# Optimization experiments

Hardware: AMD Instinct MI355X
Metric: run time of the kernel (lower is better)

Reference implementation:

```python
import jax, jax.numpy as jnp
import numpy as np

B, C, M, T = 2, 512, 16, 128
H = 8
D = C // H  # 64, divisible by 4 for 2D RoPE
G = C // 4  # GroupNorm groups = 128
S = M * T


def group_norm(x, scale, bias, groups=G, eps=1e-5):
    b, c, m, t = x.shape
    xg = x.reshape(b, groups, c // groups, m, t)
    mu = xg.mean(axis=(2, 3, 4), keepdims=True)
    var = xg.var(axis=(2, 3, 4), keepdims=True)
    xn = ((xg - mu) * jax.lax.rsqrt(var + eps)).reshape(b, c, m, t)
    return xn * scale[None, :, None, None] + bias[None, :, None, None]


def dwsep_conv(x, dw, pw):
    # depthwise 3x3 (groups=C) then pointwise 1x1
    y = jax.lax.conv_general_dilated(
        x, dw, window_strides=(1, 1), padding='SAME',
        dimension_numbers=('NCHW', 'HWIO', 'NCHW'), feature_group_count=x.shape[1])
    return jnp.einsum('bcmt,cd->bdmt', y, pw)


def rope2d(x):
    # x: [B,H,M,T,D]; first D/2 dims rotated by freq index m, last D/2 by time index t
    d = x.shape[-1]
    dh = d // 2
    q = dh // 2
    inv = 1.0 / (10000.0 ** (jnp.arange(q, dtype=jnp.float32) / q))

    def rot(v, ang):
        h = v.shape[-1] // 2
        v1, v2 = v[..., :h], v[..., h:]
        c, s = jnp.cos(ang), jnp.sin(ang)
        return jnp.concatenate([v1 * c - v2 * s, v1 * s + v2 * c], axis=-1)

    ang_f = jnp.arange(x.shape[2], dtype=jnp.float32)[:, None] * inv  # [M,q]
    ang_t = jnp.arange(x.shape[3], dtype=jnp.float32)[:, None] * inv  # [T,q]
    xf = rot(x[..., :dh], ang_f[:, None, :])  # broadcast over T
    xt = rot(x[..., dh:], ang_t)
    return jnp.concatenate([xf, xt], axis=-1)


def setup_inputs() -> dict:
    key = jax.random.key(0)
    ks = jax.random.split(key, 14)
    s = 0.02
    return {
        'x': jax.random.normal(ks[0], (B, C, M, T), jnp.float32),
        'lengths': jax.random.randint(ks[1], (B,), T // 2, T + 1),
        'gn_scale': jnp.ones((C,), jnp.float32),
        'gn_bias': jnp.zeros((C,), jnp.float32),
        'dw_q': jax.random.normal(ks[2], (3, 3, 1, C), jnp.float32) * s,
        'dw_k': jax.random.normal(ks[3], (3, 3, 1, C), jnp.float32) * s,
        'dw_v': jax.random.normal(ks[4], (3, 3, 1, C), jnp.float32) * s,
        'pw_q': jax.random.normal(ks[5], (C, C), jnp.float32) * s,
        'pw_k': jax.random.normal(ks[6], (C, C), jnp.float32) * s,
        'pw_v': jax.random.normal(ks[7], (C, C), jnp.float32) * s,
        'attn_w': jax.random.normal(ks[8], (C, C), jnp.float32) * s,
        'attn_b': jnp.zeros((C,), jnp.float32),
        'out_w': jax.random.normal(ks[9], (C, C), jnp.float32) * s,
        'out_b': jnp.zeros((C,), jnp.float32),
    }


def reference(x, lengths, gn_scale, gn_bias, dw_q, dw_k, dw_v, pw_q, pw_k, pw_v,
              attn_w, attn_b, out_w, out_b):
    residual = x
    xn = group_norm(x, gn_scale, gn_bias)

    def to_heads(y):  # [B,C,M,T] -> [B,H,M,T,D]
        return y.reshape(B, H, D, M, T).transpose(0, 1, 3, 4, 2)

    q = rope2d(to_heads(dwsep_conv(xn, dw_q, pw_q)))
    k = rope2d(to_heads(dwsep_conv(xn, dw_k, pw_k)))
    v = to_heads(dwsep_conv(xn, dw_v, pw_v))

    q = q.reshape(B, H, S, D)
    k = k.reshape(B, H, S, D)
    v = v.reshape(B, H, S, D)

    scores = jnp.einsum('bhsd,bhkd->bhsk', q, k) / np.sqrt(D).astype(np.float32)
    valid_t = jnp.arange(T)[None, :] < lengths[:, None]        # [B,T]
    valid = jnp.tile(valid_t, (1, M))                          # [B,S], token idx = m*T + t
    scores = jnp.where(valid[:, None, None, :], scores, jnp.float32(-1e9))
    attn = jax.nn.softmax(scores, axis=-1)
    o = jnp.einsum('bhsk,bhkd->bhsd', attn, v)                 # [B,H,S,D]

    o = o.transpose(0, 2, 1, 3).reshape(B, S, C)
    o = o @ attn_w + attn_b                                    # block output proj
    o = o.reshape(B, M, T, C).transpose(0, 3, 1, 2)            # [B,C,M,T]
    out = jnp.einsum('bcmt,cd->bdmt', o, out_w) + out_b[None, :, None, None]
    return residual + out
```

## Files before the change

### kernel.cpp

```cpp
#include <hip/hip_runtime.h>
#include <math.h>

#define CCH 512
#define SSQ 2048
#define MTOT 4096

typedef __bf16 bf16;
typedef __bf16 bf16x8 __attribute__((ext_vector_type(8)));
typedef __bf16 bf16x4 __attribute__((ext_vector_type(4)));
typedef float  f32x4  __attribute__((ext_vector_type(4)));

#define AS1 __attribute__((address_space(1)))
#define AS3 __attribute__((address_space(3)))
__device__ __forceinline__ void glds16(const void* g, void* l) {
    __builtin_amdgcn_global_load_lds((const AS1 void*)g, (AS3 void*)l, 16, 0, 0);
}

__global__ __launch_bounds__(256) void gnw_kernel(const float* __restrict__ x,
        float* __restrict__ mu, float* __restrict__ rstd,
        const float* __restrict__ w0, const float* __restrict__ w1,
        const float* __restrict__ w2, const float* __restrict__ w3,
        const float* __restrict__ w4, bf16* __restrict__ wT,
        const float* __restrict__ attnb, const float* __restrict__ outb,
        float* __restrict__ bcv) {
    __shared__ float smem[64*65];
    int tid = threadIdx.x;
    if (blockIdx.x < 256) {
        float* s_sum = smem;
        float* s_sq  = smem + 256;
        int bg = blockIdx.x;
        long base = (long)bg * 8192;
        float sum = 0.f, sq = 0.f;
#pragma unroll
        for (int r = 0; r < 32; ++r) {
            float v = x[base + r*256 + tid];
            sum += v; sq += v*v;
        }
        s_sum[tid] = sum; s_sq[tid] = sq;
        __syncthreads();
        for (int off = 128; off > 0; off >>= 1) {
            if (tid < off) { s_sum[tid] += s_sum[tid+off]; s_sq[tid] += s_sq[tid+off]; }
            __syncthreads();
        }
        if (tid == 0) {
            float m = s_sum[0] * (1.f/8192.f);
            float v = s_sq[0]  * (1.f/8192.f) - m*m;
            mu[bg] = m;
            rstd[bg] = rsqrtf(v + 1e-5f);
        }
    } else if (blockIdx.x < 576) {
        int bid = blockIdx.x - 256;
        int z = bid >> 6, r2 = bid & 63;
        int k0 = (r2 >> 3)*64, n0 = (r2 & 7)*64;
        const float* srcs[5] = {w0, w1, w2, w3, w4};
        const float* W = srcs[z];
        bf16* D = wT + (long)z * (CCH*CCH);
        float (*t)[65] = (float(*)[65])smem;
        int cI = tid & 63, r4 = tid >> 6;
#pragma unroll
        for (int p = 0; p < 16; ++p) {
            int kr = p*4 + r4;
            t[kr][cI] = W[(long)(k0+kr)*CCH + n0 + cI];
        }
        __syncthreads();
#pragma unroll
        for (int p = 0; p < 16; ++p) {
            int nr = p*4 + r4;
            D[(long)(n0+nr)*CCH + k0 + cI] = (bf16)t[cI][nr];
        }
    } else if (blockIdx.x < 578) {
        int n = (blockIdx.x - 576)*256 + tid;
        float a = outb[n];
#pragma unroll 16
        for (int j = 0; j < 512; ++j)
            a = fmaf(attnb[j], w4[(long)j*CCH + n], a);
        bcv[n] = a;
    } else {
        bf16* wAc = wT + (long)5*CCH*CCH;
        int base = (blockIdx.x - 578)*4096 + tid;
#pragma unroll
        for (int p = 0; p < 16; ++p)
            wAc[base + p*256] = (bf16)w3[base + p*256];
    }
}

__global__ void tn_kernel(const float* __restrict__ x, const float* __restrict__ mu,
                          const float* __restrict__ rstd, const float* __restrict__ gsc,
                          const float* __restrict__ gbs, bf16* __restrict__ xnT) {
    __shared__ float t[64][65];
    int s0 = blockIdx.x*64, c0 = blockIdx.y*64, b = blockIdx.z;
    int tid = threadIdx.x;
    int cI = tid & 63, r4 = tid >> 6;
#pragma unroll
    for (int p = 0; p < 16; ++p) {
        int cr = p*4 + r4;
        t[cr][cI] = x[((long)(b*CCH + c0 + cr))*SSQ + s0 + cI];
    }
    __syncthreads();
#pragma unroll
    for (int p = 0; p < 16; ++p) {
        int sr = p*4 + r4;
        int c = c0 + cI;
        int g = b*128 + (c >> 2);
        float v = (t[cI][sr] - mu[g]) * rstd[g] * gsc[c] + gbs[c];
        xnT[((long)(b*SSQ + s0 + sr))*CCH + c] = (bf16)v;
    }
}

__global__ __launch_bounds__(256) void dw3_kernel(const bf16* __restrict__ xnT,
        const float* __restrict__ dwq, const float* __restrict__ dwk,
        const float* __restrict__ dwv,
        bf16* __restrict__ yq, bf16* __restrict__ yk, bf16* __restrict__ yv) {
    int tid = threadIdx.x;
    int cc = (tid & 63) * 8;
    int s  = blockIdx.x*4 + (tid >> 6);
    int sl = s & (SSQ-1);
    int b  = s >> 11;
    int m = sl >> 7, t = sl & 127;
    float aq[8] = {}, ak[8] = {}, av[8] = {};
#pragma unroll
    for (int di = 0; di < 3; ++di) {
        int m2 = m + di - 1;
        if ((unsigned)m2 >= 16u) continue;
#pragma unroll
        for (int dj = 0; dj < 3; ++dj) {
            int t2 = t + dj - 1;
            if ((unsigned)t2 >= 128u) continue;
            bf16x8 xv = *(const bf16x8*)(xnT + ((long)(b*SSQ + m2*128 + t2))*CCH + cc);
            int wi = (di*3 + dj)*CCH + cc;
#pragma unroll
            for (int i = 0; i < 8; ++i) {
                float xf = (float)xv[i];
                aq[i] += xf * dwq[wi+i];
                ak[i] += xf * dwk[wi+i];
                av[i] += xf * dwv[wi+i];
            }
        }
    }
    bf16x8 oq, ok, ov;
#pragma unroll
    for (int i = 0; i < 8; ++i) { oq[i] = (bf16)aq[i]; ok[i] = (bf16)ak[i]; ov[i] = (bf16)av[i]; }
    long o = (long)s*CCH + cc;
    *(bf16x8*)(yq + o) = oq;
    *(bf16x8*)(yk + o) = ok;
    *(bf16x8*)(yv + o) = ov;
}

template<int NFR>
__device__ __forceinline__ void gemm_core128(const bf16* __restrict__ A,
        const bf16* __restrict__ Wt, int m0, int n0,
        bf16* As, bf16* Bs, f32x4 (&acc)[4][NFR]) {
    int tid = threadIdx.x, lane = tid & 63, wid = tid >> 6;
    int sw = wid & 1, nw = wid >> 1;
    int col = lane & 15, quad = lane >> 4;
    const char* gA[4]; char* ldsA[4];
#pragma unroll
    for (int p = 0; p < 4; ++p) {
        int ci = tid + p*256;
        int row = ci >> 3;
        int c = (ci & 7) ^ (row & 7);
        gA[p] = (const char*)A + ((long)(m0+row)*CCH + c*8)*2;
        ldsA[p] = (char*)As + ci*16;
    }
    const char* gB[NFR]; char* ldsB[NFR];
#pragma unroll
    for (int p = 0; p < NFR; ++p) {
        int ci = tid + p*256;
        int row = ci >> 3;
        int c = (ci & 7) ^ (row & 7);
        gB[p] = (const char*)Wt + ((long)(n0+row)*CCH + c*8)*2;
        ldsB[p] = (char*)Bs + ci*16;
    }
    int rowA = sw*64 + col;
    int rowB = nw*(NFR*16) + col;
    for (int k0 = 0; k0 < CCH; k0 += 64) {
        __syncthreads();
#pragma unroll
        for (int p = 0; p < 4; ++p)   glds16(gA[p] + k0*2, ldsA[p]);
#pragma unroll
        for (int p = 0; p < NFR; ++p) glds16(gB[p] + k0*2, ldsB[p]);
        __syncthreads();
        bf16x8 af[4][2], bfr[NFR][2];
#pragma unroll
        for (int mt = 0; mt < 4; ++mt) {
            int r = rowA + mt*16;
#pragma unroll
            for (int ks = 0; ks < 2; ++ks) {
                int c = (ks*4 + quad) ^ (r & 7);
                af[mt][ks] = *(const bf16x8*)((char*)As + r*128 + c*16);
            }
        }
#pragma unroll
        for (int nt = 0; nt < NFR; ++nt) {
            int r = rowB + nt*16;
#pragma unroll
            for (int ks = 0; ks < 2; ++ks) {
                int c = (ks*4 + quad) ^ (r & 7);
                bfr[nt][ks] = *(const bf16x8*)((char*)Bs + r*128 + c*16);
            }
        }
#pragma unroll
        for (int ks = 0; ks < 2; ++ks)
#pragma unroll
            for (int mt = 0; mt < 4; ++mt)
#pragma unroll
                for (int nt = 0; nt < NFR; ++nt)
                    acc[mt][nt] = __builtin_amdgcn_mfma_f32_16x16x32_bf16(
                        af[mt][ks], bfr[nt][ks], acc[mt][nt], 0,0,0);
    }
}

__global__ __launch_bounds__(256) void gemm_qkv(const bf16* __restrict__ Abase,
        bf16* __restrict__ wT, bf16* __restrict__ qout,
        bf16* __restrict__ kout, bf16* __restrict__ vout) {
    __shared__ bf16 As[128*64];
    __shared__ bf16 Bs[128*64];
    int z = blockIdx.z;
    if (z == 3 && blockIdx.x >= 4) return;
    int m0 = blockIdx.x*128, n0 = blockIdx.y*128;
    const bf16* Aop = (z < 3) ? Abase + (long)z*MTOT*CCH : wT + (long)4*CCH*CCH;
    const bf16* Wop = (z < 3) ? wT + (long)z*CCH*CCH   : wT + (long)5*CCH*CCH;
    f32x4 acc[4][4] = {};
    gemm_core128<4>(Aop, Wop, m0, n0, As, Bs, acc);
    int tid = threadIdx.x, lane = tid & 63, wid = tid >> 6;
    int sw = wid & 1, nw = wid >> 1;
    int col = lane & 15, quad = lane >> 4;
    int nbase = n0 + nw*64;
    int mb = m0 + sw*64;
    if (z == 3) {
        bf16* wCt = wT + (long)6*CCH*CCH;
#pragma unroll
        for (int nt = 0; nt < 4; ++nt) {
            int n = nbase + nt*16 + col;
#pragma unroll
            for (int mt = 0; mt < 4; ++mt)
#pragma unroll
                for (int r = 0; r < 4; ++r)
                    wCt[(long)(mb + mt*16 + quad*4 + r)*CCH + n] = (bf16)acc[mt][nt][r];
        }
    } else if (z < 2) {
        bf16* outp = z ? kout : qout;
        const float sc = z ? 1.0f : 0.125f;
        float invf = __expf(-(float)col * 0.5756462732485114f);
#pragma unroll
        for (int mt = 0; mt < 4; ++mt)
#pragma unroll
            for (int r = 0; r < 4; ++r) {
                int row = mb + mt*16 + quad*4 + r;
                int sl = row & (SSQ-1);
#pragma unroll
                for (int half = 0; half < 2; ++half) {
                    float pos = half ? (float)(sl & 127) : (float)(sl >> 7);
                    float ang = pos * invf;
                    float sn, cs;
                    __sincosf(ang, &sn, &cs);
                    float x1 = acc[mt][half*2+0][r], x2 = acc[mt][half*2+1][r];
                    outp[(long)row*CCH + nbase + half*32 + col]      = (bf16)((x1*cs - x2*sn)*sc);
                    outp[(long)row*CCH + nbase + half*32 + 16 + col] = (bf16)((x1*sn + x2*cs)*sc);
                }
            }
    } else {
#pragma unroll
        for (int mt = 0; mt < 4; ++mt)
#pragma unroll
            for (int nt = 0; nt < 4; ++nt) {
                int n = nbase + nt*16 + col;
                int row0 = mb + mt*16 + quad*4;
                int bq = row0 >> 11, sl0 = row0 & (SSQ-1);
                int sub16 = (sl0 >> 4) & 1;
                long slp = (long)(sl0 & ~31) + quad*8 + sub16*4;
                bf16x4 pk;
#pragma unroll
                for (int r = 0; r < 4; ++r) pk[r] = (bf16)acc[mt][nt][r];
                *(bf16x4*)(vout + ((long)(bq*CCH + n))*SSQ + slp) = pk;
            }
    }
}

__global__ __launch_bounds__(256) void gemm_out(const bf16* __restrict__ A,
        const bf16* __restrict__ Wt, const float* __restrict__ bias,
        const float* __restrict__ resid, float* __restrict__ outp) {
    __shared__ bf16 As[128*64];
    __shared__ bf16 Bs[64*64];
    int m0 = blockIdx.x*128, n0 = blockIdx.y*64;
    f32x4 acc[4][2] = {};
    gemm_core128<2>(A, Wt, m0, n0, As, Bs, acc);
    int tid = threadIdx.x, lane = tid & 63, wid = tid >> 6;
    int sw = wid & 1, nw = wid >> 1;
    int col = lane & 15, quad = lane >> 4;
    int nb = n0 + nw*32, mb = m0 + sw*64;
#pragma unroll
    for (int mt = 0; mt < 4; ++mt)
#pragma unroll
        for (int nt = 0; nt < 2; ++nt) {
            int n = nb + nt*16 + col;
            float bv = bias[n];
            int row0 = mb + mt*16 + quad*4;
            int b = row0 >> 11, sl0 = row0 & (SSQ-1);
            long off = ((long)(b*CCH + n))*SSQ + sl0;
            float4 rr = *(const float4*)(resid + off);
            float4 o4;
            o4.x = acc[mt][nt][0] + bv + rr.x;
            o4.y = acc[mt][nt][1] + bv + rr.y;
            o4.z = acc[mt][nt][2] + bv + rr.z;
            o4.w = acc[mt][nt][3] + bv + rr.w;
            *(float4*)(outp + off) = o4;
        }
}

__global__ __launch_bounds__(256, 2) void attn_kernel(
        const bf16* __restrict__ qb, const bf16* __restrict__ kb,
        const bf16* __restrict__ vb, const int* __restrict__ lengths,
        bf16* __restrict__ o) {
    __shared__ char KVs[2][32768];
    __shared__ float Lsm[4][4][16];
    int bid = blockIdx.x;
    int bh = bid & 15, qtb = bid >> 4;
    int b = bh >> 3, h = bh & 7;
    int tid = threadIdx.x, wid = tid >> 6, lane = tid & 63;
    int col = lane & 15, quad = lane >> 4;
    int q0 = qtb*64;
    int lenb = lengths[b];
    int thr = lenb - wid*32 - quad*4;

    const char* gK[4]; const char* gV[4];
#pragma unroll
    for (int j = 0; j < 4; ++j) {
        int s = j*64 + lane;
        int rl = s >> 3;
        int cin = s & 7;
        int csrc = cin ^ (rl & 7);
        gK[j] = (const char*)kb + ((long)(b*SSQ + wid*32 + rl))*1024 + h*128 + csrc*16;
        gV[j] = (const char*)vb + ((long)(b*CCH + h*64 + j*16 + col))*4096 + (wid*4 + quad)*16;
    }
    char* ldsK = (char*)KVs + wid*4096 + lane*16;
    char* ldsV = (char*)KVs + 16384 + wid*4096 + lane*16;

    const bf16* qp = qb + (long)(b*SSQ)*CCH + h*64;
    bf16x8 qf[4][2];
#pragma unroll
    for (int qt = 0; qt < 4; ++qt)
#pragma unroll
        for (int dc = 0; dc < 2; ++dc)
            qf[qt][dc] = *(const bf16x8*)(qp + (long)(q0 + qt*16 + col)*CCH + dc*32 + quad*8);

    f32x4 of[4][4] = {};
    float ls[4] = {};
    int cswz7 = col & 7;
    int kc0 = (quad ^ cswz7)*16;
    int kc1 = ((4 + quad) ^ cswz7)*16;

#pragma unroll
    for (int j = 0; j < 4; ++j) glds16(gK[j], ldsK + j*1024);
#pragma unroll
    for (int j = 0; j < 4; ++j) glds16(gV[j], ldsV + j*1024);
#pragma unroll
    for (int j = 0; j < 4; ++j) glds16(gK[j] + 131072L, ldsK + 32768 + j*1024);
#pragma unroll
    for (int j = 0; j < 4; ++j) glds16(gV[j] + 256L, ldsV + 32768 + j*1024);

    for (int t = 0; t < 16; ++t) {
        if (t == 15) { asm volatile("s_waitcnt vmcnt(0)" ::: "memory"); }
        else         { asm volatile("s_waitcnt vmcnt(8)" ::: "memory"); }
        __builtin_amdgcn_sched_barrier(0);
        const char* K = KVs[t & 1] + wid*4096;
        const char* V = KVs[t & 1] + 16384 + wid*4096;
        bf16x8 kf[2][2], vf[4];
#pragma unroll
        for (int sub = 0; sub < 2; ++sub) {
            kf[sub][0] = *(const bf16x8*)(K + sub*2048 + col*128 + kc0);
            kf[sub][1] = *(const bf16x8*)(K + sub*2048 + col*128 + kc1);
        }
#pragma unroll
        for (int dt = 0; dt < 4; ++dt)
            vf[dt] = *(const bf16x8*)(V + dt*1024 + lane*16);
        asm volatile("s_waitcnt lgkmcnt(0)" ::: "memory");
        __builtin_amdgcn_sched_barrier(0);
        if (t < 14) {
            int bsel = (t & 1)*32768;
#pragma unroll
            for (int j = 0; j < 4; ++j) glds16(gK[j] + (long)(t+2)*131072, ldsK + bsel + j*1024);
#pragma unroll
            for (int j = 0; j < 4; ++j) glds16(gV[j] + (long)(t+2)*256,    ldsV + bsel + j*1024);
        }
        __builtin_amdgcn_sched_barrier(0);
        f32x4 sc[2][4];
#pragma unroll
        for (int sub = 0; sub < 2; ++sub) {
            f32x4 m;
#pragma unroll
            for (int r = 0; r < 4; ++r) m[r] = (sub*16 + r < thr) ? 0.f : -10000.f;
#pragma unroll
            for (int qt = 0; qt < 4; ++qt) sc[sub][qt] = m;
        }
        __builtin_amdgcn_s_setprio(1);
#pragma unroll
        for (int sub = 0; sub < 2; ++sub)
#pragma unroll
            for (int qt = 0; qt < 4; ++qt) {
                sc[sub][qt] = __builtin_amdgcn_mfma_f32_16x16x32_bf16(kf[sub][0], qf[qt][0], sc[sub][qt], 0,0,0);
                sc[sub][qt] = __builtin_amdgcn_mfma_f32_16x16x32_bf16(kf[sub][1], qf[qt][1], sc[sub][qt], 0,0,0);
            }
        __builtin_amdgcn_s_setprio(0);
        bf16x8 pf[4];
#pragma unroll
        for (int qt = 0; qt < 4; ++qt) {
            float s = 0.f;
#pragma unroll
            for (int r = 0; r < 4; ++r) {
                float e0 = __expf(sc[0][qt][r]);
                float e1 = __expf(sc[1][qt][r]);
                pf[qt][r]     = (bf16)e0;
                pf[qt][4 + r] = (bf16)e1;
                s += e0 + e1;
            }
            ls[qt] += s;
        }
        __builtin_amdgcn_s_setprio(1);
#pragma unroll
        for (int dt = 0; dt < 4; ++dt)
#pragma unroll
            for (int qt = 0; qt < 4; ++qt)
                of[qt][dt] = __builtin_amdgcn_mfma_f32_16x16x32_bf16(pf[qt], vf[dt], of[qt][dt], 0,0,0);
        __builtin_amdgcn_s_setprio(0);
    }

#pragma unroll
    for (int qt = 0; qt < 4; ++qt) {
        ls[qt] += __shfl_xor(ls[qt], 16);
        ls[qt] += __shfl_xor(ls[qt], 32);
    }
    __syncthreads();
    float* Om = (float*)KVs;
#pragma unroll
    for (int qt = 0; qt < 4; ++qt)
#pragma unroll
        for (int dt = 0; dt < 4; ++dt)
#pragma unroll
            for (int r = 0; r < 4; ++r)
                Om[(wid*64 + qt*16 + quad*4 + r)*64 + dt*16 + col] = of[qt][dt][r];
    if (quad == 0)
#pragma unroll
        for (int qt = 0; qt < 4; ++qt) Lsm[wid][qt][col] = ls[qt];
    __syncthreads();
    bf16* ob = o + (long)(b*SSQ + q0)*CCH + h*64;
#pragma unroll
    for (int i = 0; i < 16; ++i) {
        int rr = wid*16 + i;
        float v = Om[rr*64 + lane] + Om[(64 + rr)*64 + lane]
                + Om[(128 + rr)*64 + lane] + Om[(192 + rr)*64 + lane];
        float l = Lsm[0][wid][i] + Lsm[1][wid][i] + Lsm[2][wid][i] + Lsm[3][wid][i];
        ob[(long)rr*CCH + lane] = (bf16)(v / l);
    }
}

extern "C" void kernel_launch(void* const* d_in, const int* in_sizes, int n_in,
                              void* d_out, int out_size, void* d_ws, size_t ws_size,
                              hipStream_t stream) {
    const float* x        = (const float*)d_in[0];
    const int*   lengths  = (const int*)  d_in[1];
    const float* gn_scale = (const float*)d_in[2];
    const float* gn_bias  = (const float*)d_in[3];
    const float* dw_q     = (const float*)d_in[4];
    const float* dw_k     = (const float*)d_in[5];
    const float* dw_v     = (const float*)d_in[6];
    const float* pw_q     = (const float*)d_in[7];
    const float* pw_k     = (const float*)d_in[8];
    const float* pw_v     = (const float*)d_in[9];
    const float* attn_w   = (const float*)d_in[10];
    const float* attn_b   = (const float*)d_in[11];
    const float* out_w    = (const float*)d_in[12];
    const float* out_b    = (const float*)d_in[13];
    float* out = (float*)d_out;

    char* w = (char*)d_ws;
    float* mu   = (float*)w;
    float* rstd = (float*)(w + 1024);
    float* bcv  = (float*)(w + 2048);
    bf16* wT    = (bf16*)(w + 4096);
    bf16* wCt = wT + (long)6*CCH*CCH;
    bf16* xnT  = (bf16*)(w + 0x00400000);
    bf16* yT   = (bf16*)(w + 0x00800000);
    bf16* qbf  = (bf16*)(w + 0x01400000);
    bf16* kbf  = (bf16*)(w + 0x01800000);
    bf16* vbf  = (bf16*)(w + 0x01C00000);
    bf16* obf  = (bf16*)(w + 0x02000000);

    gnw_kernel<<<642, 256, 0, stream>>>(x, mu, rstd, pw_q, pw_k, pw_v, attn_w, out_w,
                                        wT, attn_b, out_b, bcv);
    tn_kernel<<<dim3(32,8,2), 256, 0, stream>>>(x, mu, rstd, gn_scale, gn_bias, xnT);
    dw3_kernel<<<MTOT/4, 256, 0, stream>>>(xnT, dw_q, dw_k, dw_v,
                                           yT, yT + (long)MTOT*CCH, yT + (long)2*MTOT*CCH);

    gemm_qkv<<<dim3(MTOT/128, CCH/128, 4), 256, 0, stream>>>(yT, wT, qbf, kbf, vbf);

    attn_kernel<<<512, 256, 0, stream>>>(qbf, kbf, vbf, lengths, obf);

    gemm_out<<<dim3(MTOT/128, CCH/64), 256, 0, stream>>>(obf, wCt, bcv, x, out);
}
```

Baseline: 162.6 us.

## Load V tiles straight into registers and halve attention LDS footprint

```diff
diff --git a/kernel.cpp b/kernel.cpp
--- a/kernel.cpp
+++ b/kernel.cpp
@@ -14,6 +14,9 @@
 #define AS3 __attribute__((address_space(3)))
 __device__ __forceinline__ void glds16(const void* g, void* l) {
     __builtin_amdgcn_global_load_lds((const AS1 void*)g, (AS3 void*)l, 16, 0, 0);
+}
+__device__ __forceinline__ float fexp2(float x) {
+    float r; asm("v_exp_f32 %0, %1" : "=v"(r) : "v"(x)); return r;
 }
 
 __global__ __launch_bounds__(256) void gnw_kernel(const float* __restrict__ x,
@@ -240,7 +243,7 @@
         }
     } else if (z < 2) {
         bf16* outp = z ? kout : qout;
-        const float sc = z ? 1.0f : 0.125f;
+        const float sc = z ? 1.0f : 0.18033688f;
         float invf = __expf(-(float)col * 0.5756462732485114f);
 #pragma unroll
         for (int mt = 0; mt < 4; ++mt)
@@ -308,11 +311,79 @@
         }
 }
 
+__device__ __forceinline__ void attn_tile12(int t, const char* ldsKr, char* ldsK,
+        const char* const (&gK)[4], const char* const (&gV)[4],
+        const bf16x8 (&qf)[4][2], int thr, int col, int quad, int kc0, int kc1,
+        bf16x8 (&vCur)[4], bf16x8 (&vNxt)[4], f32x4 (&of)[4][4], float (&ls)[4]) {
+    if (t == 15) { asm volatile("s_waitcnt vmcnt(4)" ::: "memory"); }
+    else         { asm volatile("s_waitcnt vmcnt(8)" ::: "memory"); }
+    __builtin_amdgcn_sched_barrier(0);
+    const char* K = ldsKr + (t & 1)*16384;
+    bf16x8 kf[2][2];
+#pragma unroll
+    for (int sub = 0; sub < 2; ++sub) {
+        kf[sub][0] = *(const bf16x8*)(K + sub*2048 + col*128 + kc0);
+        kf[sub][1] = *(const bf16x8*)(K + sub*2048 + col*128 + kc1);
+    }
+    asm volatile("s_waitcnt lgkmcnt(0)" ::: "memory");
+    __builtin_amdgcn_sched_barrier(0);
+    if (t < 14) {
+#pragma unroll
+        for (int j = 0; j < 4; ++j)
+            glds16(gK[j] + (long)(t+2)*131072, ldsK + (t & 1)*16384 + j*1024);
+    }
+    if (t < 15) {
+#pragma unroll
+        for (int j = 0; j < 4; ++j)
+            vNxt[j] = *(const bf16x8*)(gV[j] + (long)(t+1)*256);
+    }
+    __builtin_amdgcn_sched_barrier(0);
+    f32x4 sc[2][4];
+#pragma unroll
+    for (int sub = 0; sub < 2; ++sub) {
+        f32x4 m;
+#pragma unroll
+        for (int r = 0; r < 4; ++r) m[r] = (sub*16 + r < thr) ? 0.f : -10000.f;
+#pragma unroll
+        for (int qt = 0; qt < 4; ++qt) sc[sub][qt] = m;
+    }
+    __builtin_amdgcn_s_setprio(1);
+#pragma unroll
+    for (int sub = 0; sub < 2; ++sub)
+#pragma unroll
+        for (int qt = 0; qt < 4; ++qt) {
+            sc[sub][qt] = __builtin_amdgcn_mfma_f32_16x16x32_bf16(kf[sub][0], qf[qt][0], sc[sub][qt], 0,0,0);
+            sc[sub][qt] = __builtin_amdgcn_mfma_f32_16x16x32_bf16(kf[sub][1], qf[qt][1], sc[sub][qt], 0,0,0);
+        }
+    __builtin_amdgcn_s_setprio(0);
+    bf16x8 pf[4];
+#pragma unroll
+    for (int qt = 0; qt < 4; ++qt) {
+        float s = 0.f;
+#pragma unroll
+        for (int r = 0; r < 4; ++r) {
+            float e0 = fexp2(sc[0][qt][r]);
+            float e1 = fexp2(sc[1][qt][r]);
+            pf[qt][r]     = (bf16)e0;
+            pf[qt][4 + r] = (bf16)e1;
+            s += e0 + e1;
+        }
+        ls[qt] += s;
+    }
+    __builtin_amdgcn_s_setprio(1);
+#pragma unroll
+    for (int dt = 0; dt < 4; ++dt)
+#pragma unroll
+        for (int qt = 0; qt < 4; ++qt)
+            of[qt][dt] = __builtin_amdgcn_mfma_f32_16x16x32_bf16(pf[qt], vCur[dt], of[qt][dt], 0,0,0);
+    __builtin_amdgcn_s_setprio(0);
+}
+
 __global__ __launch_bounds__(256, 2) void attn_kernel(
         const bf16* __restrict__ qb, const bf16* __restrict__ kb,
         const bf16* __restrict__ vb, const int* __restrict__ lengths,
         bf16* __restrict__ o) {
-    __shared__ char KVs[2][32768];
+    __shared__ char Ks[2][16384];
     __shared__ float Lsm[4][4][16];
     int bid = blockIdx.x;
     int bh = bid & 15, qtb = bid >> 4;
@@ -333,8 +404,8 @@
         gK[j] = (const char*)kb + ((long)(b*SSQ + wid*32 + rl))*1024 + h*128 + csrc*16;
         gV[j] = (const char*)vb + ((long)(b*CCH + h*64 + j*16 + col))*4096 + (wid*4 + quad)*16;
     }
-    char* ldsK = (char*)KVs + wid*4096 + lane*16;
-    char* ldsV = (char*)KVs + 16384 + wid*4096 + lane*16;
+    char* ldsK = (char*)Ks + wid*4096 + lane*16;
+    const char* ldsKr = (const char*)Ks + wid*4096;
 
     const bf16* qp = qb + (long)(b*SSQ)*CCH + h*64;
     bf16x8 qf[4][2];
@@ -350,79 +421,17 @@
     int kc0 = (quad ^ cswz7)*16;
     int kc1 = ((4 + quad) ^ cswz7)*16;
 
+    bf16x8 vA[4], vB[4];
 #pragma unroll
     for (int j = 0; j < 4; ++j) glds16(gK[j], ldsK + j*1024);
 #pragma unroll
-    for (int j = 0; j < 4; ++j) glds16(gV[j], ldsV + j*1024);
-#pragma unroll
-    for (int j = 0; j < 4; ++j) glds16(gK[j] + 131072L, ldsK + 32768 + j*1024);
-#pragma unroll
-    for (int j = 0; j < 4; ++j) glds16(gV[j] + 256L, ldsV + 32768 + j*1024);
-
-    for (int t = 0; t < 16; ++t) {
-        if (t == 15) { asm volatile("s_waitcnt vmcnt(0)" ::: "memory"); }
-        else         { asm volatile("s_waitcnt vmcnt(8)" ::: "memory"); }
-        __builtin_amdgcn_sched_barrier(0);
-        const char* K = KVs[t & 1] + wid*4096;
-        const char* V = KVs[t & 1] + 16384 + wid*4096;
-        bf16x8 kf[2][2], vf[4];
-#pragma unroll
-        for (int sub = 0; sub < 2; ++sub) {
-            kf[sub][0] = *(const bf16x8*)(K + sub*2048 + col*128 + kc0);
-            kf[sub][1] = *(const bf16x8*)(K + sub*2048 + col*128 + kc1);
-        }
-#pragma unroll
-        for (int dt = 0; dt < 4; ++dt)
-            vf[dt] = *(const bf16x8*)(V + dt*1024 + lane*16);
-        asm volatile("s_waitcnt lgkmcnt(0)" ::: "memory");
-        __builtin_amdgcn_sched_barrier(0);
-        if (t < 14) {
-            int bsel = (t & 1)*32768;
-#pragma unroll
-            for (int j = 0; j < 4; ++j) glds16(gK[j] + (long)(t+2)*131072, ldsK + bsel + j*1024);
-#pragma unroll
-            for (int j = 0; j < 4; ++j) glds16(gV[j] + (long)(t+2)*256,    ldsV + bsel + j*1024);
-        }
-        __builtin_amdgcn_sched_barrier(0);
-        f32x4 sc[2][4];
-#pragma unroll
-        for (int sub = 0; sub < 2; ++sub) {
-            f32x4 m;
-#pragma unroll
-            for (int r = 0; r < 4; ++r) m[r] = (sub*16 + r < thr) ? 0.f : -10000.f;
-#pragma unroll
-            for (int qt = 0; qt < 4; ++qt) sc[sub][qt] = m;
-        }
-        __builtin_amdgcn_s_setprio(1);
-#pragma unroll
-        for (int sub = 0; sub < 2; ++sub)
-#pragma unroll
-            for (int qt = 0; qt < 4; ++qt) {
-                sc[sub][qt] = __builtin_amdgcn_mfma_f32_16x16x32_bf16(kf[sub][0], qf[qt][0], sc[sub][qt], 0,0,0);
-                sc[sub][qt] = __builtin_amdgcn_mfma_f32_16x16x32_bf16(kf[sub][1], qf[qt][1], sc[sub][qt], 0,0,0);
-            }
-        __builtin_amdgcn_s_setprio(0);
-        bf16x8 pf[4];
-#pragma unroll
-        for (int qt = 0; qt < 4; ++qt) {
-            float s = 0.f;
-#pragma unroll
-            for (int r = 0; r < 4; ++r) {
-                float e0 = __expf(sc[0][qt][r]);
-                float e1 = __expf(sc[1][qt][r]);
-                pf[qt][r]     = (bf16)e0;
-                pf[qt][4 + r] = (bf16)e1;
-                s += e0 + e1;
-            }
-            ls[qt] += s;
-        }
-        __builtin_amdgcn_s_setprio(1);
-#pragma unroll
-        for (int dt = 0; dt < 4; ++dt)
-#pragma unroll
-            for (int qt = 0; qt < 4; ++qt)
-                of[qt][dt] = __builtin_amdgcn_mfma_f32_16x16x32_bf16(pf[qt], vf[dt], of[qt][dt], 0,0,0);
-        __builtin_amdgcn_s_setprio(0);
+    for (int j = 0; j < 4; ++j) glds16(gK[j] + 131072L, ldsK + 16384 + j*1024);
+#pragma unroll
+    for (int j = 0; j < 4; ++j) vA[j] = *(const bf16x8*)(gV[j]);
+
+    for (int t2 = 0; t2 < 16; t2 += 2) {
+        attn_tile12(t2,     ldsKr, ldsK, gK, gV, qf, thr, col, quad, kc0, kc1, vA, vB, of, ls);
+        attn_tile12(t2 + 1, ldsKr, ldsK, gK, gV, qf, thr, col, quad, kc0, kc1, vB, vA, of, ls);
     }
 
 #pragma unroll
@@ -431,26 +440,32 @@
         ls[qt] += __shfl_xor(ls[qt], 32);
     }
     __syncthreads();
-    float* Om = (float*)KVs;
-#pragma unroll
-    for (int qt = 0; qt < 4; ++qt)
-#pragma unroll
-        for (int dt = 0; dt < 4; ++dt)
-#pragma unroll
-            for (int r = 0; r < 4; ++r)
-                Om[(wid*64 + qt*16 + quad*4 + r)*64 + dt*16 + col] = of[qt][dt][r];
-    if (quad == 0)
-#pragma unroll
-        for (int qt = 0; qt < 4; ++qt) Lsm[wid][qt][col] = ls[qt];
-    __syncthreads();
+    float* Om = (float*)Ks;
     bf16* ob = o + (long)(b*SSQ + q0)*CCH + h*64;
-#pragma unroll
-    for (int i = 0; i < 16; ++i) {
-        int rr = wid*16 + i;
-        float v = Om[rr*64 + lane] + Om[(64 + rr)*64 + lane]
-                + Om[(128 + rr)*64 + lane] + Om[(192 + rr)*64 + lane];
-        float l = Lsm[0][wid][i] + Lsm[1][wid][i] + Lsm[2][wid][i] + Lsm[3][wid][i];
-        ob[(long)rr*CCH + lane] = (bf16)(v / l);
+    int dl = lane & 31, rh = lane >> 5;
+#pragma unroll
+    for (int p = 0; p < 2; ++p) {
+        if (p) __syncthreads();
+#pragma unroll
+        for (int qt = 0; qt < 4; ++qt)
+#pragma unroll
+            for (int dtl = 0; dtl < 2; ++dtl)
+#pragma unroll
+                for (int r = 0; r < 4; ++r)
+                    Om[(wid*64 + qt*16 + quad*4 + r)*32 + dtl*16 + col] = of[qt][p*2 + dtl][r];
+        if (p == 0 && quad == 0)
+#pragma unroll
+            for (int qt = 0; qt < 4; ++qt) Lsm[wid][qt][col] = ls[qt];
+        __syncthreads();
+#pragma unroll
+        for (int it = 0; it < 8; ++it) {
+            int rr = wid*16 + it*2 + rh;
+            float v = Om[rr*32 + dl] + Om[(64 + rr)*32 + dl]
+                    + Om[(128 + rr)*32 + dl] + Om[(192 + rr)*32 + dl];
+            float l = Lsm[0][rr>>4][rr&15] + Lsm[1][rr>>4][rr&15]
+                    + Lsm[2][rr>>4][rr&15] + Lsm[3][rr>>4][rr&15];
+            ob[(long)rr*CCH + p*32 + dl] = (bf16)(v / l);
+        }
     }
 }
 
```

After: 164.1 us. Within noise of the previous version (+0.9%).
